# Kernel optimization log

Hardware: AMD Instinct MI355X
Metric: run time of the kernel (lower is better)

## Reference

```python
import jax, jax.numpy as jnp
import numpy as np
import math

L = 3        # n_layers
H = 8        # n_heads
D = 128      # embed_dim
KD = D // H  # key_dim = val_dim = 16
FF = 512     # feed_forward_hidden
B, N = 200, 100
BN = B * N
E = 320000
EPS = 1e-5   # BatchNorm1d eps


def setup_inputs() -> dict:
    key = jax.random.key(0)
    ks = jax.random.split(key, 12)

    def u(k, shape, last):  # torch uniform(-1/sqrt(last), 1/sqrt(last)) init
        s = 1.0 / math.sqrt(last)
        return jax.random.uniform(k, shape, jnp.float32, -s, s)

    x = jax.random.normal(ks[0], (B, N, D), jnp.float32)
    edge_index = jax.random.randint(ks[1], (2, E), 0, BN, jnp.int32)
    return {
        "x": x,
        "edge_index": edge_index,
        "Wq": u(ks[2], (L, H, D, KD), KD),
        "Wk": u(ks[3], (L, H, D, KD), KD),
        "Wv": u(ks[4], (L, H, D, KD), KD),
        "Wout": u(ks[5], (L, H, KD, D), D),
        "bn1_w": jnp.ones((L, D), jnp.float32),
        "bn1_b": jnp.zeros((L, D), jnp.float32),
        "W1": u(ks[6], (L, D, FF), D),
        "b1": u(ks[7], (L, FF), D),
        "W2": u(ks[8], (L, FF, D), FF),
        "b2": u(ks[9], (L, D), FF),
        "bn2_w": jnp.ones((L, D), jnp.float32),
        "bn2_b": jnp.zeros((L, D), jnp.float32),
    }


def _batch_norm(h, w, b):
    # BatchNorm1d over flattened (B*N, D), training-mode batch stats (biased var)
    flat = h.reshape(-1, h.shape[-1])
    mu = flat.mean(axis=0)
    var = flat.var(axis=0)
    y = (flat - mu) / jnp.sqrt(var + EPS) * w + b
    return y.reshape(h.shape)


def _gat_conv(h, src, dst, Wq, Wk, Wv, Wout):
    Bb, Nn, Dd = h.shape
    bn = Bb * Nn
    flat = h.reshape(bn, Dd)
    Hh, _, Kk = Wq.shape
    # faithful to torch: matmul gives [H, BN, K], then raw .view(BN, H, K)
    Q = jnp.einsum('nd,hdk->hnk', flat, Wq).reshape(bn, Hh, Kk)
    Kt = jnp.einsum('nd,hdk->hnk', flat, Wk).reshape(bn, Hh, Kk)
    V = jnp.einsum('nd,hdk->hnk', flat, Wv).reshape(bn, Hh, Kk)
    norm = 1.0 / math.sqrt(Kk)
    # message: Q_j (source) . K_i (target) per edge, per head -> [E, H]
    attn = norm * jnp.sum(Q[src] * Kt[dst], axis=-1)
    # segment softmax over edges grouped by target node (max detached, as in PyG)
    m = jax.lax.stop_gradient(jax.ops.segment_max(attn, dst, num_segments=bn))
    ex = jnp.exp(attn - m[dst])
    s = jax.ops.segment_sum(ex, dst, num_segments=bn)
    a = ex / (s[dst] + 1e-16)
    # weighted V_i scatter-added into target nodes -> [BN, H, K]
    aggr = jax.ops.segment_sum(V[dst] * a[:, :, None], dst, num_segments=bn)
    out = aggr.reshape(bn, Hh * Kk) @ Wout.reshape(Hh * Kk, -1)
    return out.reshape(Bb, Nn, -1)


def reference(x, edge_index, Wq, Wk, Wv, Wout, bn1_w, bn1_b, W1, b1, W2, b2, bn2_w, bn2_b):
    src, dst = edge_index[0], edge_index[1]
    h = x
    for l in range(L):
        h = h + _gat_conv(h, src, dst, Wq[l], Wk[l], Wv[l], Wout[l])
        h = _batch_norm(h, bn1_w[l], bn1_b[l])
        ff = jnp.maximum(h @ W1[l] + b1[l], 0.0) @ W2[l] + b2[l]
        h = h + ff
        h = _batch_norm(h, bn2_w[l], bn2_b[l])
    return h
```

## Files before the change

### kernel.cpp

```cpp
#include <hip/hip_runtime.h>
#include <hip/hip_bf16.h>

#define BN_ 20000
#define D_ 128
#define FF_ 512
#define E_ 320000
#define NBLK 313
#define LSTR 136

typedef __attribute__((ext_vector_type(8))) short bf16x8;
typedef __attribute__((ext_vector_type(4))) float f32x4;

__device__ __forceinline__ unsigned short f2b(float f) {
    unsigned int u = __float_as_uint(f);
    u = (u + 0x7FFFu + ((u >> 16) & 1u)) >> 16;
    return (unsigned short)u;
}

__device__ __forceinline__ void make_ss(const float* __restrict__ acc,
                                        const float* __restrict__ w,
                                        const float* __restrict__ b,
                                        float* __restrict__ ss_sh, int tid) {
    if (tid < 128) {
        if (acc) {
            float s = acc[tid], q = acc[128 + tid];
            float mu  = s * (1.f / 20000.f);
            float var = fmaxf(q * (1.f / 20000.f) - mu * mu, 0.f);
            float rstd  = rsqrtf(var + 1e-5f);
            float scale = w[tid] * rstd;
            ss_sh[tid]       = scale;
            ss_sh[128 + tid] = b[tid] - mu * scale;
        } else {
            ss_sh[tid]       = 1.f;
            ss_sh[128 + tid] = 0.f;
        }
    }
}

__global__ __launch_bounds__(256) void k_prep(const float* __restrict__ Wv,
                                              const float* __restrict__ Wout,
                                              const float* __restrict__ W1,
                                              const float* __restrict__ W2,
                                              unsigned short* __restrict__ WcT,
                                              unsigned short* __restrict__ WoT,
                                              unsigned short* __restrict__ W1T,
                                              unsigned short* __restrict__ W2T,
                                              float* __restrict__ flag) {
    int idx = blockIdx.x * 256 + threadIdx.x;
    if (idx < 49152) {
        int l = idx / 16384, r = idx % 16384;
        int n = r >> 7, k = r & 127;
        int h = n >> 4, kk = n & 15;
        WcT[idx] = f2b(Wv[((l * 8 + h) * 128 + k) * 16 + kk]);
        return;
    }
    idx -= 49152;
    if (idx < 49152) {
        int l = idx / 16384, r = idx % 16384;
        int n = r >> 7, k = r & 127;
        WoT[idx] = f2b(Wout[l * 16384 + k * 128 + n]);
        return;
    }
    idx -= 49152;
    if (idx < 196608) {
        int l = idx / 65536, r = idx % 65536;
        int n = r >> 7, k = r & 127;
        W1T[idx] = f2b(W1[l * 65536 + k * 512 + n]);
        return;
    }
    idx -= 196608;
    if (idx < 196608) {
        int l = idx / 65536, r = idx % 65536;
        int n = r / 512, k = r % 512;
        W2T[idx] = f2b(W2[l * 65536 + k * 128 + n]);
        return;
    }
    idx -= 196608;
    if (idx < 20000) flag[idx] = 0.f;
}

__global__ __launch_bounds__(256) void k_flag(const int* __restrict__ dst,
                                              float* __restrict__ flag) {
    int e = blockIdx.x * 256 + threadIdx.x;
    if (e < E_) flag[dst[e]] = 1.0f;
}


__global__ __launch_bounds__(256) void k_vs(const float* __restrict__ H,
                                            const float* __restrict__ accP,
                                            const float* __restrict__ bnw,
                                            const float* __restrict__ bnb,
                                            const unsigned short* __restrict__ Bt,
                                            unsigned short* __restrict__ Vs,
                                            float* __restrict__ accZ) {
    __shared__ unsigned short As[64 * LSTR];
    __shared__ unsigned short Bs[64 * LSTR];
    __shared__ float ss_sh[256];
    const int tid = threadIdx.x;
    const int row0 = blockIdx.x * 64, col0 = blockIdx.y * 64;
    make_ss(accP, bnw, bnb, ss_sh, tid);
    if (blockIdx.x == 0 && blockIdx.y == 0) accZ[tid] = 0.f;
    __syncthreads();
#pragma unroll
    for (int it = 0; it < 4; ++it) {
        int idx = tid + it * 256;
        int m = idx >> 4, k0 = (idx & 15) << 3;
        int gr = row0 + m;
        float v[8];
        if (gr < BN_) {
            f32x4 v0 = *(const f32x4*)(H + gr * D_ + k0);
            f32x4 v1 = *(const f32x4*)(H + gr * D_ + k0 + 4);
            v[0] = v0.x; v[1] = v0.y; v[2] = v0.z; v[3] = v0.w;
            v[4] = v1.x; v[5] = v1.y; v[6] = v1.z; v[7] = v1.w;
        } else {
#pragma unroll
            for (int j = 0; j < 8; ++j) v[j] = 0.f;
        }
        unsigned int p[4];
#pragma unroll
        for (int j = 0; j < 4; ++j) {
            unsigned short lo = f2b(v[2 * j] * ss_sh[k0 + 2 * j] + ss_sh[128 + k0 + 2 * j]);
            unsigned short hi = f2b(v[2 * j + 1] * ss_sh[k0 + 2 * j + 1] + ss_sh[128 + k0 + 2 * j + 1]);
            p[j] = (unsigned int)lo | ((unsigned int)hi << 16);
        }
        *(uint4*)&As[m * LSTR + k0] = make_uint4(p[0], p[1], p[2], p[3]);
    }
#pragma unroll
    for (int it = 0; it < 4; ++it) {
        int idx = tid + it * 256;
        int n = idx >> 4, k0 = (idx & 15) << 3;
        *(uint4*)&Bs[n * LSTR + k0] = *(const uint4*)(Bt + (col0 + n) * D_ + k0);
    }
    __syncthreads();
    const int lane = tid & 63, wave = tid >> 6;
    const int l16 = lane & 15, quad = lane >> 4;
    const int wm = (wave >> 1) * 32, wn = (wave & 1) * 32;
    f32x4 acc[2][2] = {};
#pragma unroll
    for (int kb = 0; kb < 128; kb += 32) {
        bf16x8 a0 = *(bf16x8*)&As[(wm + l16) * LSTR + kb + quad * 8];
        bf16x8 a1 = *(bf16x8*)&As[(wm + 16 + l16) * LSTR + kb + quad * 8];
        bf16x8 b0 = *(bf16x8*)&Bs[(wn + l16) * LSTR + kb + quad * 8];
        bf16x8 b1 = *(bf16x8*)&Bs[(wn + 16 + l16) * LSTR + kb + quad * 8];
        acc[0][0] = __builtin_amdgcn_mfma_f32_16x16x32_bf16(a0, b0, acc[0][0], 0, 0, 0);
        acc[0][1] = __builtin_amdgcn_mfma_f32_16x16x32_bf16(a0, b1, acc[0][1], 0, 0, 0);
        acc[1][0] = __builtin_amdgcn_mfma_f32_16x16x32_bf16(a1, b0, acc[1][0], 0, 0, 0);
        acc[1][1] = __builtin_amdgcn_mfma_f32_16x16x32_bf16(a1, b1, acc[1][1], 0, 0, 0);
    }
#pragma unroll
    for (int i = 0; i < 2; ++i)
#pragma unroll
        for (int j = 0; j < 2; ++j) {
            int gc = col0 + wn + j * 16 + l16;
            int h = gc >> 4, kk = gc & 15;
#pragma unroll
            for (int r = 0; r < 4; ++r) {
                int gr = row0 + wm + i * 16 + quad * 4 + r;
                if (gr < BN_) Vs[h * (BN_ * 16) + gr * 16 + kk] = f2b(acc[i][j][r]);
            }
        }
}

__global__ __launch_bounds__(256) void k_out(const unsigned short* __restrict__ Vs,
                                             const unsigned short* __restrict__ Bt,
                                             const float* __restrict__ H,
                                             const float* __restrict__ accP,
                                             const float* __restrict__ bnw,
                                             const float* __restrict__ bnb,
                                             const float* __restrict__ flag,
                                             float* __restrict__ H1,
                                             float* __restrict__ accA) {
    __shared__ unsigned short As[64 * LSTR];
    __shared__ unsigned short Bs[64 * LSTR];
    __shared__ float ss_sh[256];
    const int tid = threadIdx.x;
    const int row0 = blockIdx.x * 64, col0 = blockIdx.y * 64;
    make_ss(accP, bnw, bnb, ss_sh, tid);
#pragma unroll
    for (int it = 0; it < 4; ++it) {
        int idx = tid + it * 256;
        int m = idx >> 4, k0 = (idx & 15) << 3;
        int gr = row0 + m;
        uint4 w = make_uint4(0u, 0u, 0u, 0u);
        if (gr < BN_) w = *(const uint4*)(Vs + gr * D_ + k0);
        *(uint4*)&As[m * LSTR + k0] = w;
    }
#pragma unroll
    for (int it = 0; it < 4; ++it) {
        int idx = tid + it * 256;
        int n = idx >> 4, k0 = (idx & 15) << 3;
        *(uint4*)&Bs[n * LSTR + k0] = *(const uint4*)(Bt + (col0 + n) * D_ + k0);
    }
    __syncthreads();
    const int lane = tid & 63, wave = tid >> 6;
    const int l16 = lane & 15, quad = lane >> 4;
    const int wm = (wave >> 1) * 32, wn = (wave & 1) * 32;
    f32x4 acc[2][2] = {};
#pragma unroll
    for (int kb = 0; kb < 128; kb += 32) {
        bf16x8 a0 = *(bf16x8*)&As[(wm + l16) * LSTR + kb + quad * 8];
        bf16x8 a1 = *(bf16x8*)&As[(wm + 16 + l16) * LSTR + kb + quad * 8];
        bf16x8 b0 = *(bf16x8*)&Bs[(wn + l16) * LSTR + kb + quad * 8];
        bf16x8 b1 = *(bf16x8*)&Bs[(wn + 16 + l16) * LSTR + kb + quad * 8];
        acc[0][0] = __builtin_amdgcn_mfma_f32_16x16x32_bf16(a0, b0, acc[0][0], 0, 0, 0);
        acc[0][1] = __builtin_amdgcn_mfma_f32_16x16x32_bf16(a0, b1, acc[0][1], 0, 0, 0);
        acc[1][0] = __builtin_amdgcn_mfma_f32_16x16x32_bf16(a1, b0, acc[1][0], 0, 0, 0);
        acc[1][1] = __builtin_amdgcn_mfma_f32_16x16x32_bf16(a1, b1, acc[1][1], 0, 0, 0);
    }
    __syncthreads();
    float* Sred = (float*)As;
    float* Qred = (float*)Bs;
    const int slot = (wave >> 1) * 4 + quad;
#pragma unroll
    for (int j = 0; j < 2; ++j) {
        int gc = col0 + wn + j * 16 + l16;
        float sc = ss_sh[gc - col0 + ((gc >= col0) ? 0 : 0)];
        sc = ss_sh[(gc & 127)];
        float sh = ss_sh[128 + (gc & 127)];
        float cs = 0.f, cq = 0.f;
#pragma unroll
        for (int i = 0; i < 2; ++i)
#pragma unroll
            for (int r = 0; r < 4; ++r) {
                int gr = row0 + wm + i * 16 + quad * 4 + r;
                if (gr < BN_) {
                    float z = H[gr * D_ + gc] * sc + sh;
                    float o = z + flag[gr] * acc[i][j][r];
                    H1[gr * D_ + gc] = o;
                    cs += o; cq += o * o;
                }
            }
        Sred[(wn + j * 16 + l16) * 8 + slot] = cs;
        Qred[(wn + j * 16 + l16) * 8 + slot] = cq;
    }
    __syncthreads();
    if (tid < 64) {
        float s = 0.f, q = 0.f;
#pragma unroll
        for (int t = 0; t < 8; ++t) { s += Sred[tid * 8 + t]; q += Qred[tid * 8 + t]; }
        atomicAdd(&accA[col0 + tid], s);
        atomicAdd(&accA[128 + col0 + tid], q);
    }
}

__global__ __launch_bounds__(256) void k_ff1(const float* __restrict__ H1,
                                             const float* __restrict__ accA,
                                             const float* __restrict__ bnw,
                                             const float* __restrict__ bnb,
                                             const unsigned short* __restrict__ Bt,
                                             const float* __restrict__ b1l,
                                             unsigned short* __restrict__ T,
                                             float* __restrict__ accZ) {
    __shared__ unsigned short As[64 * LSTR];
    __shared__ unsigned short Bs[64 * LSTR];
    __shared__ float ss_sh[256];
    const int tid = threadIdx.x;
    const int row0 = blockIdx.x * 64, col0 = blockIdx.y * 64;
    make_ss(accA, bnw, bnb, ss_sh, tid);
    if (blockIdx.x == 0 && blockIdx.y == 0) accZ[tid] = 0.f;
    __syncthreads();
#pragma unroll
    for (int it = 0; it < 4; ++it) {
        int idx = tid + it * 256;
        int m = idx >> 4, k0 = (idx & 15) << 3;
        int gr = row0 + m;
        float v[8];
        if (gr < BN_) {
            f32x4 v0 = *(const f32x4*)(H1 + gr * D_ + k0);
            f32x4 v1 = *(const f32x4*)(H1 + gr * D_ + k0 + 4);
            v[0] = v0.x; v[1] = v0.y; v[2] = v0.z; v[3] = v0.w;
            v[4] = v1.x; v[5] = v1.y; v[6] = v1.z; v[7] = v1.w;
        } else {
#pragma unroll
            for (int j = 0; j < 8; ++j) v[j] = 0.f;
        }
        unsigned int p[4];
#pragma unroll
        for (int j = 0; j < 4; ++j) {
            unsigned short lo = f2b(v[2 * j] * ss_sh[k0 + 2 * j] + ss_sh[128 + k0 + 2 * j]);
            unsigned short hi = f2b(v[2 * j + 1] * ss_sh[k0 + 2 * j + 1] + ss_sh[128 + k0 + 2 * j + 1]);
            p[j] = (unsigned int)lo | ((unsigned int)hi << 16);
        }
        *(uint4*)&As[m * LSTR + k0] = make_uint4(p[0], p[1], p[2], p[3]);
    }
#pragma unroll
    for (int it = 0; it < 4; ++it) {
        int idx = tid + it * 256;
        int n = idx >> 4, k0 = (idx & 15) << 3;
        *(uint4*)&Bs[n * LSTR + k0] = *(const uint4*)(Bt + (col0 + n) * D_ + k0);
    }
    __syncthreads();
    const int lane = tid & 63, wave = tid >> 6;
    const int l16 = lane & 15, quad = lane >> 4;
    const int wm = (wave >> 1) * 32, wn = (wave & 1) * 32;
    f32x4 acc[2][2] = {};
#pragma unroll
    for (int kb = 0; kb < 128; kb += 32) {
        bf16x8 a0 = *(bf16x8*)&As[(wm + l16) * LSTR + kb + quad * 8];
        bf16x8 a1 = *(bf16x8*)&As[(wm + 16 + l16) * LSTR + kb + quad * 8];
        bf16x8 b0 = *(bf16x8*)&Bs[(wn + l16) * LSTR + kb + quad * 8];
        bf16x8 b1 = *(bf16x8*)&Bs[(wn + 16 + l16) * LSTR + kb + quad * 8];
        acc[0][0] = __builtin_amdgcn_mfma_f32_16x16x32_bf16(a0, b0, acc[0][0], 0, 0, 0);
        acc[0][1] = __builtin_amdgcn_mfma_f32_16x16x32_bf16(a0, b1, acc[0][1], 0, 0, 0);
        acc[1][0] = __builtin_amdgcn_mfma_f32_16x16x32_bf16(a1, b0, acc[1][0], 0, 0, 0);
        acc[1][1] = __builtin_amdgcn_mfma_f32_16x16x32_bf16(a1, b1, acc[1][1], 0, 0, 0);
    }
#pragma unroll
    for (int j = 0; j < 2; ++j) {
        int gc = col0 + wn + j * 16 + l16;
        float bb = b1l[gc];
#pragma unroll
        for (int i = 0; i < 2; ++i)
#pragma unroll
            for (int r = 0; r < 4; ++r) {
                int gr = row0 + wm + i * 16 + quad * 4 + r;
                if (gr < BN_) T[gr * FF_ + gc] = f2b(fmaxf(acc[i][j][r] + bb, 0.f));
            }
    }
}

__global__ __launch_bounds__(256) void k_ff2(const unsigned short* __restrict__ T,
                                             const unsigned short* __restrict__ Bt,
                                             const float* __restrict__ H1,
                                             const float* __restrict__ accA,
                                             const float* __restrict__ bnw,
                                             const float* __restrict__ bnb,
                                             const float* __restrict__ b2l,
                                             float* __restrict__ H2,
                                             float* __restrict__ accB) {
    __shared__ unsigned short As[64 * LSTR];
    __shared__ unsigned short Bs[64 * LSTR];
    __shared__ float ss_sh[256];
    const int tid = threadIdx.x;
    const int row0 = blockIdx.x * 64, col0 = blockIdx.y * 64;
    const int lane = tid & 63, wave = tid >> 6;
    const int l16 = lane & 15, quad = lane >> 4;
    const int wm = (wave >> 1) * 32, wn = (wave & 1) * 32;
    make_ss(accA, bnw, bnb, ss_sh, tid);
    f32x4 acc[2][2] = {};
    for (int kc = 0; kc < FF_; kc += 128) {
        if (kc) __syncthreads();
#pragma unroll
        for (int it = 0; it < 4; ++it) {
            int idx = tid + it * 256;
            int m = idx >> 4, k0 = (idx & 15) << 3;
            int gr = row0 + m;
            uint4 w = make_uint4(0u, 0u, 0u, 0u);
            if (gr < BN_) w = *(const uint4*)(T + gr * FF_ + kc + k0);
            *(uint4*)&As[m * LSTR + k0] = w;
        }
#pragma unroll
        for (int it = 0; it < 4; ++it) {
            int idx = tid + it * 256;
            int n = idx >> 4, k0 = (idx & 15) << 3;
            *(uint4*)&Bs[n * LSTR + k0] = *(const uint4*)(Bt + (col0 + n) * FF_ + kc + k0);
        }
        __syncthreads();
#pragma unroll
        for (int kb = 0; kb < 128; kb += 32) {
            bf16x8 a0 = *(bf16x8*)&As[(wm + l16) * LSTR + kb + quad * 8];
            bf16x8 a1 = *(bf16x8*)&As[(wm + 16 + l16) * LSTR + kb + quad * 8];
            bf16x8 b0 = *(bf16x8*)&Bs[(wn + l16) * LSTR + kb + quad * 8];
            bf16x8 b1 = *(bf16x8*)&Bs[(wn + 16 + l16) * LSTR + kb + quad * 8];
            acc[0][0] = __builtin_amdgcn_mfma_f32_16x16x32_bf16(a0, b0, acc[0][0], 0, 0, 0);
            acc[0][1] = __builtin_amdgcn_mfma_f32_16x16x32_bf16(a0, b1, acc[0][1], 0, 0, 0);
            acc[1][0] = __builtin_amdgcn_mfma_f32_16x16x32_bf16(a1, b0, acc[1][0], 0, 0, 0);
            acc[1][1] = __builtin_amdgcn_mfma_f32_16x16x32_bf16(a1, b1, acc[1][1], 0, 0, 0);
        }
    }
    __syncthreads();
    float* Sred = (float*)As;
    float* Qred = (float*)Bs;
    const int slot = (wave >> 1) * 4 + quad;
#pragma unroll
    for (int j = 0; j < 2; ++j) {
        int gc = col0 + wn + j * 16 + l16;
        float sc = ss_sh[gc & 127], sh = ss_sh[128 + (gc & 127)], bb = b2l[gc];
        float cs = 0.f, cq = 0.f;
#pragma unroll
        for (int i = 0; i < 2; ++i)
#pragma unroll
            for (int r = 0; r < 4; ++r) {
                int gr = row0 + wm + i * 16 + quad * 4 + r;
                if (gr < BN_) {
                    float o = H1[gr * D_ + gc] * sc + sh + acc[i][j][r] + bb;
                    H2[gr * D_ + gc] = o;
                    cs += o; cq += o * o;
                }
            }
        Sred[(wn + j * 16 + l16) * 8 + slot] = cs;
        Qred[(wn + j * 16 + l16) * 8 + slot] = cq;
    }
    __syncthreads();
    if (tid < 64) {
        float s = 0.f, q = 0.f;
#pragma unroll
        for (int t = 0; t < 8; ++t) { s += Sred[tid * 8 + t]; q += Qred[tid * 8 + t]; }
        atomicAdd(&accB[col0 + tid], s);
        atomicAdd(&accB[128 + col0 + tid], q);
    }
}

__global__ __launch_bounds__(256) void k_apply(const float4* __restrict__ H2,
                                               const float* __restrict__ accB,
                                               const float* __restrict__ bnw,
                                               const float* __restrict__ bnb,
                                               float4* __restrict__ out) {
    __shared__ float ss_sh[256];
    make_ss(accB, bnw, bnb, ss_sh, threadIdx.x);
    __syncthreads();
    int i = blockIdx.x * 256 + threadIdx.x;
    if (i >= BN_ * D_ / 4) return;
    int c = (i & 31) << 2;
    float4 v = H2[i];
    v.x = v.x * ss_sh[c + 0] + ss_sh[128 + c + 0];
    v.y = v.y * ss_sh[c + 1] + ss_sh[128 + c + 1];
    v.z = v.z * ss_sh[c + 2] + ss_sh[128 + c + 2];
    v.w = v.w * ss_sh[c + 3] + ss_sh[128 + c + 3];
    out[i] = v;
}


extern "C" void kernel_launch(void* const* d_in, const int* in_sizes, int n_in,
                              void* d_out, int out_size, void* d_ws, size_t ws_size,
                              hipStream_t stream) {
    (void)in_sizes; (void)n_in; (void)out_size; (void)ws_size;
    const float* x    = (const float*)d_in[0];
    const int*   edge = (const int*)d_in[1];
    const float* Wv   = (const float*)d_in[4];
    const float* Wout = (const float*)d_in[5];
    const float* bn1w = (const float*)d_in[6];
    const float* bn1b = (const float*)d_in[7];
    const float* W1   = (const float*)d_in[8];
    const float* b1   = (const float*)d_in[9];
    const float* W2   = (const float*)d_in[10];
    const float* b2   = (const float*)d_in[11];
    const float* bn2w = (const float*)d_in[12];
    const float* bn2b = (const float*)d_in[13];

    float* ws   = (float*)d_ws;
    float* bufA = ws;
    float* bufB = ws + 2560000;
    float* flag = ws + 5120000;
    float* accA = ws + 5140000;
    float* accB = ws + 5140256;
    unsigned short* Vs  = (unsigned short*)(ws + 5140512);
    unsigned short* T   = (unsigned short*)(ws + 6420512);
    unsigned short* WcT = (unsigned short*)(ws + 11540512);
    unsigned short* WoT = (unsigned short*)(ws + 11565088);
    unsigned short* W1T = (unsigned short*)(ws + 11589664);
    unsigned short* W2T = (unsigned short*)(ws + 11687968);

    k_prep<<<1999, 256, 0, stream>>>(Wv, Wout, W1, W2, WcT, WoT, W1T, W2T, flag);
    k_flag<<<1250, 256, 0, stream>>>(edge + E_, flag);

    for (int l = 0; l < 3; ++l) {
        const float* Hc   = (l == 0) ? x : bufA;
        const float* accP = (l == 0) ? nullptr : accB;
        const float* bw   = bn2w + (l ? (l - 1) * 128 : 0);
        const float* bbv  = bn2b + (l ? (l - 1) * 128 : 0);
        k_vs<<<dim3(NBLK, 2), 256, 0, stream>>>(Hc, accP, bw, bbv,
                                                WcT + l * 16384, Vs, accA);
        k_out<<<dim3(NBLK, 2), 256, 0, stream>>>(Vs, WoT + l * 16384, Hc, accP,
                                                 bw, bbv, flag, bufB, accA);
        k_ff1<<<dim3(NBLK, 8), 256, 0, stream>>>(bufB, accA, bn1w + l * 128,
                                                 bn1b + l * 128, W1T + l * 65536,
                                                 b1 + l * 512, T, accB);
        k_ff2<<<dim3(NBLK, 2), 256, 0, stream>>>(T, W2T + l * 65536, bufB, accA,
                                                 bn1w + l * 128, bn1b + l * 128,
                                                 b2 + l * 128, bufA, accB);
    }
    k_apply<<<2500, 256, 0, stream>>>((const float4*)bufA, accB, bn2w + 256,
                                      bn2b + 256, (float4*)d_out);
}
```

Before: 297.9 us.

## Fuse FF1 and FF2 into one kernel keeping hidden activations in LDS

```diff
diff --git a/kernel.cpp b/kernel.cpp
--- a/kernel.cpp
+++ b/kernel.cpp
@@ -7,6 +7,8 @@
 #define E_ 320000
 #define NBLK 313
 #define LSTR 136
+#define TSTR 72
+#define B2STR 72
 
 typedef __attribute__((ext_vector_type(8))) short bf16x8;
 typedef __attribute__((ext_vector_type(4))) float f32x4;
@@ -45,7 +47,8 @@
                                               unsigned short* __restrict__ WoT,
                                               unsigned short* __restrict__ W1T,
                                               unsigned short* __restrict__ W2T,
-                                              float* __restrict__ flag) {
+                                              float* __restrict__ flag,
+                                              float* __restrict__ acc6) {
     int idx = blockIdx.x * 256 + threadIdx.x;
     if (idx < 49152) {
         int l = idx / 16384, r = idx % 16384;
@@ -76,7 +79,9 @@
         return;
     }
     idx -= 196608;
-    if (idx < 20000) flag[idx] = 0.f;
+    if (idx < 20000) { flag[idx] = 0.f; return; }
+    idx -= 20000;
+    if (idx < 1536) acc6[idx] = 0.f;
 }
 
 __global__ __launch_bounds__(256) void k_flag(const int* __restrict__ dst,
@@ -91,15 +96,13 @@
                                             const float* __restrict__ bnw,
                                             const float* __restrict__ bnb,
                                             const unsigned short* __restrict__ Bt,
-                                            unsigned short* __restrict__ Vs,
-                                            float* __restrict__ accZ) {
+                                            unsigned short* __restrict__ Vs) {
     __shared__ unsigned short As[64 * LSTR];
     __shared__ unsigned short Bs[64 * LSTR];
     __shared__ float ss_sh[256];
     const int tid = threadIdx.x;
     const int row0 = blockIdx.x * 64, col0 = blockIdx.y * 64;
     make_ss(accP, bnw, bnb, ss_sh, tid);
-    if (blockIdx.x == 0 && blockIdx.y == 0) accZ[tid] = 0.f;
     __syncthreads();
 #pragma unroll
     for (int it = 0; it < 4; ++it) {
@@ -169,7 +172,7 @@
                                              const float* __restrict__ bnb,
                                              const float* __restrict__ flag,
                                              float* __restrict__ H1,
-                                             float* __restrict__ accA) {
+                                             float* __restrict__ accO) {
     __shared__ unsigned short As[64 * LSTR];
     __shared__ unsigned short Bs[64 * LSTR];
     __shared__ float ss_sh[256];
@@ -214,8 +217,7 @@
 #pragma unroll
     for (int j = 0; j < 2; ++j) {
         int gc = col0 + wn + j * 16 + l16;
-        float sc = ss_sh[gc - col0 + ((gc >= col0) ? 0 : 0)];
-        sc = ss_sh[(gc & 127)];
+        float sc = ss_sh[gc & 127];
         float sh = ss_sh[128 + (gc & 127)];
         float cs = 0.f, cq = 0.f;
 #pragma unroll
@@ -238,26 +240,29 @@
         float s = 0.f, q = 0.f;
 #pragma unroll
         for (int t = 0; t < 8; ++t) { s += Sred[tid * 8 + t]; q += Qred[tid * 8 + t]; }
-        atomicAdd(&accA[col0 + tid], s);
-        atomicAdd(&accA[128 + col0 + tid], q);
-    }
-}
-
-__global__ __launch_bounds__(256) void k_ff1(const float* __restrict__ H1,
-                                             const float* __restrict__ accA,
-                                             const float* __restrict__ bnw,
-                                             const float* __restrict__ bnb,
-                                             const unsigned short* __restrict__ Bt,
-                                             const float* __restrict__ b1l,
-                                             unsigned short* __restrict__ T,
-                                             float* __restrict__ accZ) {
+        atomicAdd(&accO[col0 + tid], s);
+        atomicAdd(&accO[128 + col0 + tid], q);
+    }
+}
+
+__global__ __launch_bounds__(256) void k_ff(const float* __restrict__ H1,
+                                            const float* __restrict__ accP,
+                                            const float* __restrict__ bnw,
+                                            const float* __restrict__ bnb,
+                                            const unsigned short* __restrict__ W1t,
+                                            const float* __restrict__ b1l,
+                                            const unsigned short* __restrict__ W2t,
+                                            const float* __restrict__ b2l,
+                                            float* __restrict__ H2,
+                                            float* __restrict__ accO) {
     __shared__ unsigned short As[64 * LSTR];
     __shared__ unsigned short Bs[64 * LSTR];
+    __shared__ unsigned short B2[128 * B2STR];
+    __shared__ unsigned short Tch[64 * TSTR];
     __shared__ float ss_sh[256];
     const int tid = threadIdx.x;
-    const int row0 = blockIdx.x * 64, col0 = blockIdx.y * 64;
-    make_ss(accA, bnw, bnb, ss_sh, tid);
-    if (blockIdx.x == 0 && blockIdx.y == 0) accZ[tid] = 0.f;
+    const int row0 = blockIdx.x * 64;
+    make_ss(accP, bnw, bnb, ss_sh, tid);
     __syncthreads();
 #pragma unroll
     for (int it = 0; it < 4; ++it) {
@@ -283,89 +288,62 @@
         }
         *(uint4*)&As[m * LSTR + k0] = make_uint4(p[0], p[1], p[2], p[3]);
     }
-#pragma unroll
-    for (int it = 0; it < 4; ++it) {
-        int idx = tid + it * 256;
-        int n = idx >> 4, k0 = (idx & 15) << 3;
-        *(uint4*)&Bs[n * LSTR + k0] = *(const uint4*)(Bt + (col0 + n) * D_ + k0);
-    }
-    __syncthreads();
     const int lane = tid & 63, wave = tid >> 6;
     const int l16 = lane & 15, quad = lane >> 4;
-    const int wm = (wave >> 1) * 32, wn = (wave & 1) * 32;
-    f32x4 acc[2][2] = {};
-#pragma unroll
-    for (int kb = 0; kb < 128; kb += 32) {
-        bf16x8 a0 = *(bf16x8*)&As[(wm + l16) * LSTR + kb + quad * 8];
-        bf16x8 a1 = *(bf16x8*)&As[(wm + 16 + l16) * LSTR + kb + quad * 8];
-        bf16x8 b0 = *(bf16x8*)&Bs[(wn + l16) * LSTR + kb + quad * 8];
-        bf16x8 b1 = *(bf16x8*)&Bs[(wn + 16 + l16) * LSTR + kb + quad * 8];
-        acc[0][0] = __builtin_amdgcn_mfma_f32_16x16x32_bf16(a0, b0, acc[0][0], 0, 0, 0);
-        acc[0][1] = __builtin_amdgcn_mfma_f32_16x16x32_bf16(a0, b1, acc[0][1], 0, 0, 0);
-        acc[1][0] = __builtin_amdgcn_mfma_f32_16x16x32_bf16(a1, b0, acc[1][0], 0, 0, 0);
-        acc[1][1] = __builtin_amdgcn_mfma_f32_16x16x32_bf16(a1, b1, acc[1][1], 0, 0, 0);
-    }
-#pragma unroll
-    for (int j = 0; j < 2; ++j) {
-        int gc = col0 + wn + j * 16 + l16;
-        float bb = b1l[gc];
-#pragma unroll
-        for (int i = 0; i < 2; ++i)
-#pragma unroll
-            for (int r = 0; r < 4; ++r) {
-                int gr = row0 + wm + i * 16 + quad * 4 + r;
-                if (gr < BN_) T[gr * FF_ + gc] = f2b(fmaxf(acc[i][j][r] + bb, 0.f));
-            }
-    }
-}
-
-__global__ __launch_bounds__(256) void k_ff2(const unsigned short* __restrict__ T,
-                                             const unsigned short* __restrict__ Bt,
-                                             const float* __restrict__ H1,
-                                             const float* __restrict__ accA,
-                                             const float* __restrict__ bnw,
-                                             const float* __restrict__ bnb,
-                                             const float* __restrict__ b2l,
-                                             float* __restrict__ H2,
-                                             float* __restrict__ accB) {
-    __shared__ unsigned short As[64 * LSTR];
-    __shared__ unsigned short Bs[64 * LSTR];
-    __shared__ float ss_sh[256];
-    const int tid = threadIdx.x;
-    const int row0 = blockIdx.x * 64, col0 = blockIdx.y * 64;
-    const int lane = tid & 63, wave = tid >> 6;
-    const int l16 = lane & 15, quad = lane >> 4;
-    const int wm = (wave >> 1) * 32, wn = (wave & 1) * 32;
-    make_ss(accA, bnw, bnb, ss_sh, tid);
-    f32x4 acc[2][2] = {};
-    for (int kc = 0; kc < FF_; kc += 128) {
-        if (kc) __syncthreads();
-#pragma unroll
-        for (int it = 0; it < 4; ++it) {
-            int idx = tid + it * 256;
-            int m = idx >> 4, k0 = (idx & 15) << 3;
-            int gr = row0 + m;
-            uint4 w = make_uint4(0u, 0u, 0u, 0u);
-            if (gr < BN_) w = *(const uint4*)(T + gr * FF_ + kc + k0);
-            *(uint4*)&As[m * LSTR + k0] = w;
-        }
+    const int wm = (wave >> 1) * 32;
+    const int wn = (wave & 1) * 32;
+    const int wn2 = (wave & 1) * 64;
+    f32x4 acc2[2][4] = {};
+    for (int c = 0; c < 8; ++c) {
+        const int cb = c * 64;
+        __syncthreads();
 #pragma unroll
         for (int it = 0; it < 4; ++it) {
             int idx = tid + it * 256;
             int n = idx >> 4, k0 = (idx & 15) << 3;
-            *(uint4*)&Bs[n * LSTR + k0] = *(const uint4*)(Bt + (col0 + n) * FF_ + kc + k0);
+            *(uint4*)&Bs[n * LSTR + k0] = *(const uint4*)(W1t + (cb + n) * D_ + k0);
+        }
+#pragma unroll
+        for (int it = 0; it < 4; ++it) {
+            int idx = tid + it * 256;
+            int n = idx >> 3, k0 = (idx & 7) << 3;
+            *(uint4*)&B2[n * B2STR + k0] = *(const uint4*)(W2t + n * FF_ + cb + k0);
         }
         __syncthreads();
+        f32x4 acc1[2][2] = {};
 #pragma unroll
         for (int kb = 0; kb < 128; kb += 32) {
             bf16x8 a0 = *(bf16x8*)&As[(wm + l16) * LSTR + kb + quad * 8];
             bf16x8 a1 = *(bf16x8*)&As[(wm + 16 + l16) * LSTR + kb + quad * 8];
             bf16x8 b0 = *(bf16x8*)&Bs[(wn + l16) * LSTR + kb + quad * 8];
             bf16x8 b1 = *(bf16x8*)&Bs[(wn + 16 + l16) * LSTR + kb + quad * 8];
-            acc[0][0] = __builtin_amdgcn_mfma_f32_16x16x32_bf16(a0, b0, acc[0][0], 0, 0, 0);
-            acc[0][1] = __builtin_amdgcn_mfma_f32_16x16x32_bf16(a0, b1, acc[0][1], 0, 0, 0);
-            acc[1][0] = __builtin_amdgcn_mfma_f32_16x16x32_bf16(a1, b0, acc[1][0], 0, 0, 0);
-            acc[1][1] = __builtin_amdgcn_mfma_f32_16x16x32_bf16(a1, b1, acc[1][1], 0, 0, 0);
+            acc1[0][0] = __builtin_amdgcn_mfma_f32_16x16x32_bf16(a0, b0, acc1[0][0], 0, 0, 0);
+            acc1[0][1] = __builtin_amdgcn_mfma_f32_16x16x32_bf16(a0, b1, acc1[0][1], 0, 0, 0);
+            acc1[1][0] = __builtin_amdgcn_mfma_f32_16x16x32_bf16(a1, b0, acc1[1][0], 0, 0, 0);
+            acc1[1][1] = __builtin_amdgcn_mfma_f32_16x16x32_bf16(a1, b1, acc1[1][1], 0, 0, 0);
+        }
+#pragma unroll
+        for (int j = 0; j < 2; ++j) {
+            int lc = wn + j * 16 + l16;
+            float bb = b1l[cb + lc];
+#pragma unroll
+            for (int i = 0; i < 2; ++i)
+#pragma unroll
+                for (int r = 0; r < 4; ++r)
+                    Tch[(wm + i * 16 + quad * 4 + r) * TSTR + lc] =
+                        f2b(fmaxf(acc1[i][j][r] + bb, 0.f));
+        }
+        __syncthreads();
+#pragma unroll
+        for (int kb = 0; kb < 64; kb += 32) {
+            bf16x8 a0 = *(bf16x8*)&Tch[(wm + l16) * TSTR + kb + quad * 8];
+            bf16x8 a1 = *(bf16x8*)&Tch[(wm + 16 + l16) * TSTR + kb + quad * 8];
+#pragma unroll
+            for (int j2 = 0; j2 < 4; ++j2) {
+                bf16x8 b = *(bf16x8*)&B2[(wn2 + j2 * 16 + l16) * B2STR + kb + quad * 8];
+                acc2[0][j2] = __builtin_amdgcn_mfma_f32_16x16x32_bf16(a0, b, acc2[0][j2], 0, 0, 0);
+                acc2[1][j2] = __builtin_amdgcn_mfma_f32_16x16x32_bf16(a1, b, acc2[1][j2], 0, 0, 0);
+            }
         }
     }
     __syncthreads();
@@ -373,9 +351,9 @@
     float* Qred = (float*)Bs;
     const int slot = (wave >> 1) * 4 + quad;
 #pragma unroll
-    for (int j = 0; j < 2; ++j) {
-        int gc = col0 + wn + j * 16 + l16;
-        float sc = ss_sh[gc & 127], sh = ss_sh[128 + (gc & 127)], bb = b2l[gc];
+    for (int j2 = 0; j2 < 4; ++j2) {
+        int gc = wn2 + j2 * 16 + l16;
+        float sc = ss_sh[gc], sh = ss_sh[128 + gc], bb = b2l[gc];
         float cs = 0.f, cq = 0.f;
 #pragma unroll
         for (int i = 0; i < 2; ++i)
@@ -383,31 +361,31 @@
             for (int r = 0; r < 4; ++r) {
                 int gr = row0 + wm + i * 16 + quad * 4 + r;
                 if (gr < BN_) {
-                    float o = H1[gr * D_ + gc] * sc + sh + acc[i][j][r] + bb;
+                    float o = H1[gr * D_ + gc] * sc + sh + acc2[i][j2][r] + bb;
                     H2[gr * D_ + gc] = o;
                     cs += o; cq += o * o;
                 }
             }
-        Sred[(wn + j * 16 + l16) * 8 + slot] = cs;
-        Qred[(wn + j * 16 + l16) * 8 + slot] = cq;
-    }
-    __syncthreads();
-    if (tid < 64) {
+        Sred[gc * 8 + slot] = cs;
+        Qred[gc * 8 + slot] = cq;
+    }
+    __syncthreads();
+    if (tid < 128) {
         float s = 0.f, q = 0.f;
 #pragma unroll
         for (int t = 0; t < 8; ++t) { s += Sred[tid * 8 + t]; q += Qred[tid * 8 + t]; }
-        atomicAdd(&accB[col0 + tid], s);
-        atomicAdd(&accB[128 + col0 + tid], q);
+        atomicAdd(&accO[tid], s);
+        atomicAdd(&accO[128 + tid], q);
     }
 }
 
 __global__ __launch_bounds__(256) void k_apply(const float4* __restrict__ H2,
-                                               const float* __restrict__ accB,
+                                               const float* __restrict__ accP,
                                                const float* __restrict__ bnw,
                                                const float* __restrict__ bnb,
                                                float4* __restrict__ out) {
     __shared__ float ss_sh[256];
-    make_ss(accB, bnw, bnb, ss_sh, threadIdx.x);
+    make_ss(accP, bnw, bnb, ss_sh, threadIdx.x);
     __syncthreads();
     int i = blockIdx.x * 256 + threadIdx.x;
     if (i >= BN_ * D_ / 4) return;
@@ -442,34 +420,32 @@
     float* bufA = ws;
     float* bufB = ws + 2560000;
     float* flag = ws + 5120000;
-    float* accA = ws + 5140000;
-    float* accB = ws + 5140256;
-    unsigned short* Vs  = (unsigned short*)(ws + 5140512);
-    unsigned short* T   = (unsigned short*)(ws + 6420512);
-    unsigned short* WcT = (unsigned short*)(ws + 11540512);
-    unsigned short* WoT = (unsigned short*)(ws + 11565088);
-    unsigned short* W1T = (unsigned short*)(ws + 11589664);
-    unsigned short* W2T = (unsigned short*)(ws + 11687968);
-
-    k_prep<<<1999, 256, 0, stream>>>(Wv, Wout, W1, W2, WcT, WoT, W1T, W2T, flag);
+    float* acc6 = ws + 5140000;
+    unsigned short* Vs  = (unsigned short*)(ws + 5141536);
+    unsigned short* WcT = (unsigned short*)(ws + 6421536);
+    unsigned short* WoT = (unsigned short*)(ws + 6446112);
+    unsigned short* W1T = (unsigned short*)(ws + 6470688);
+    unsigned short* W2T = (unsigned short*)(ws + 6568992);
+
+    k_prep<<<2005, 256, 0, stream>>>(Wv, Wout, W1, W2, WcT, WoT, W1T, W2T,
+                                     flag, acc6);
     k_flag<<<1250, 256, 0, stream>>>(edge + E_, flag);
 
     for (int l = 0; l < 3; ++l) {
         const float* Hc   = (l == 0) ? x : bufA;
-        const float* accP = (l == 0) ? nullptr : accB;
-        const float* bw   = bn2w + (l ? (l - 1) * 128 : 0);
-        const float* bbv  = bn2b + (l ? (l - 1) * 128 : 0);
+        const float* accP = (l == 0) ? nullptr : acc6 + (2 * l - 1) * 256;
+        float* acc1p = acc6 + (2 * l) * 256;
+        float* acc2p = acc6 + (2 * l + 1) * 256;
+        const float* bw  = bn2w + (l ? (l - 1) * 128 : 0);
+        const float* bbv = bn2b + (l ? (l - 1) * 128 : 0);
         k_vs<<<dim3(NBLK, 2), 256, 0, stream>>>(Hc, accP, bw, bbv,
-                                                WcT + l * 16384, Vs, accA);
+                                                WcT + l * 16384, Vs);
         k_out<<<dim3(NBLK, 2), 256, 0, stream>>>(Vs, WoT + l * 16384, Hc, accP,
-                                                 bw, bbv, flag, bufB, accA);
-        k_ff1<<<dim3(NBLK, 8), 256, 0, stream>>>(bufB, accA, bn1w + l * 128,
-                                                 bn1b + l * 128, W1T + l * 65536,
-                                                 b1 + l * 512, T, accB);
-        k_ff2<<<dim3(NBLK, 2), 256, 0, stream>>>(T, W2T + l * 65536, bufB, accA,
-                                                 bn1w + l * 128, bn1b + l * 128,
-                                                 b2 + l * 128, bufA, accB);
-    }
-    k_apply<<<2500, 256, 0, stream>>>((const float4*)bufA, accB, bn2w + 256,
-                                      bn2b + 256, (float4*)d_out);
-}
+                                                 bw, bbv, flag, bufB, acc1p);
+        k_ff<<<NBLK, 256, 0, stream>>>(bufB, acc1p, bn1w + l * 128, bn1b + l * 128,
+                                       W1T + l * 65536, b1 + l * 512,
+                                       W2T + l * 65536, b2 + l * 128, bufA, acc2p);
+    }
+    k_apply<<<2500, 256, 0, stream>>>((const float4*)bufA, acc6 + 5 * 256,
+                                      bn2w + 256, bn2b + 256, (float4*)d_out);
+}
```

Result: faster. 251.4 us (-15.6%).
